# Kernel tuning notes

Hardware: AMD Instinct MI355X
Metric: run time of the kernel (lower is better)

The kernel has to match this reference:

```python
import jax, jax.numpy as jnp
import numpy as np

D_MODEL = 3072
NUM_EXPERTS = 8
TOP_K = 2
BATCH, SEQ = 4, 4096


def setup_inputs() -> dict:
    key = jax.random.key(0)
    kx, kw, kb = jax.random.split(key, 3)
    x = jax.random.normal(kx, (BATCH, SEQ, D_MODEL), dtype=jnp.float32)
    W = jax.random.normal(kw, (NUM_EXPERTS, D_MODEL), dtype=jnp.float32) * (1.0 / np.sqrt(D_MODEL))
    b = jax.random.normal(kb, (NUM_EXPERTS,), dtype=jnp.float32) * 0.02
    return {"x": x, "W": W, "b": b}


def reference(x, W, b):
    # Linear gate: [B, S, D] x [E, D]^T -> [B, S, E]
    logits = jnp.einsum("bsd,ed->bse", x, W) + b
    gate_scores = jax.nn.softmax(logits, axis=-1)
    # top-k over experts
    topk_values, topk_indices = jax.lax.top_k(gate_scores, TOP_K)
    # renormalize the selected scores with a second softmax
    topk_values = jax.nn.softmax(topk_values, axis=-1)
    return (topk_values, topk_indices)
```

## Files before the change

kernel.cpp:

```cpp
#include <hip/hip_runtime.h>
#include <stdint.h>


#define NTOK   16384
#define DMODEL 3072
#define NEXP   8
#define NDB    8
#define DCH    (DMODEL / NDB)
#define DS     32
#define NST    (DCH / DS)
#define TPB    256

__global__ __launch_bounds__(TPB) void gate_logits_kernel(
    const float* __restrict__ x, const float* __restrict__ W,
    float* __restrict__ part) {
  __shared__ float sw[NEXP * DCH];

  const int tid = threadIdx.x;
  const int wv = tid >> 6;
  const int lane = tid & 63;
  const int sl = lane >> 3;
  const int tg = lane & 7;
  const int tokBase = blockIdx.x * TPB;
  const int dBase = blockIdx.y * DCH;

  for (int f = tid; f < NEXP * DCH / 4; f += TPB) {
    const int e = f / (DCH / 4);
    const int j = f - e * (DCH / 4);
    *(float4*)&sw[e * DCH + j * 4] =
        *(const float4*)&W[e * DMODEL + dBase + j * 4];
  }
  __syncthreads();

  const float* p8[8];
#pragma unroll
  for (int p = 0; p < 8; ++p)
    p8[p] = x + (size_t)(tokBase + wv * 64 + p * 8 + tg) * DMODEL + dBase +
            sl * 4;

  float acc[8][NEXP];
#pragma unroll
  for (int p = 0; p < 8; ++p)
#pragma unroll
    for (int e = 0; e < NEXP; ++e) acc[p][e] = 0.f;

  float4 xa[8], xb[8];
#pragma unroll
  for (int p = 0; p < 8; ++p) xa[p] = *(const float4*)(p8[p]);

#pragma unroll 1
  for (int s = 0; s < NST; s += 2) {
#pragma unroll
    for (int p = 0; p < 8; ++p)
      xb[p] = *(const float4*)(p8[p] + (s + 1) * DS);

    float4 w4[NEXP];
#pragma unroll
    for (int e = 0; e < NEXP; ++e)
      w4[e] = *(const float4*)&sw[e * DCH + s * DS + sl * 4];

#pragma unroll
    for (int p = 0; p < 8; ++p) {
      const float4 xv = xa[p];
#pragma unroll
      for (int e = 0; e < NEXP; ++e)
        acc[p][e] = fmaf(xv.x, w4[e].x,
                    fmaf(xv.y, w4[e].y,
                    fmaf(xv.z, w4[e].z,
                    fmaf(xv.w, w4[e].w, acc[p][e]))));
    }

    if (s + 2 < NST) {
#pragma unroll
      for (int p = 0; p < 8; ++p)
        xa[p] = *(const float4*)(p8[p] + (s + 2) * DS);
    }

#pragma unroll
    for (int e = 0; e < NEXP; ++e)
      w4[e] = *(const float4*)&sw[e * DCH + (s + 1) * DS + sl * 4];

#pragma unroll
    for (int p = 0; p < 8; ++p) {
      const float4 xv = xb[p];
#pragma unroll
      for (int e = 0; e < NEXP; ++e)
        acc[p][e] = fmaf(xv.x, w4[e].x,
                    fmaf(xv.y, w4[e].y,
                    fmaf(xv.z, w4[e].z,
                    fmaf(xv.w, w4[e].w, acc[p][e]))));
    }
  }

#pragma unroll
  for (int p = 0; p < 8; ++p)
#pragma unroll
    for (int e = 0; e < NEXP; ++e) {
      float v = acc[p][e];
      v += __shfl_xor(v, 8, 64);
      v += __shfl_xor(v, 16, 64);
      v += __shfl_xor(v, 32, 64);
      acc[p][e] = v;
    }

  float out8[NEXP];
#pragma unroll
  for (int p = 0; p < 8; ++p) {
    if (p == sl) {
#pragma unroll
      for (int e = 0; e < NEXP; ++e) out8[e] = acc[p][e];
    }
  }

  float* op =
      part + ((size_t)blockIdx.y * NTOK + tokBase + wv * 64 + lane) * NEXP;
  *(float4*)op = make_float4(out8[0], out8[1], out8[2], out8[3]);
  *(float4*)(op + 4) = make_float4(out8[4], out8[5], out8[6], out8[7]);
}

__global__ __launch_bounds__(64) void gate_topk_kernel(
    const float* __restrict__ part, const float* __restrict__ bias,
    float* __restrict__ out) {
  const int t = blockIdx.x * 64 + threadIdx.x;
  if (t >= NTOK) return;

  float l[NEXP];
#pragma unroll
  for (int e = 0; e < NEXP; ++e) l[e] = bias[e];
#pragma unroll
  for (int p = 0; p < NDB; ++p) {
    const float* pp = &part[(size_t)p * NTOK * NEXP + (size_t)t * NEXP];
    const float4 a = *(const float4*)pp;
    const float4 b = *(const float4*)(pp + 4);
    l[0] += a.x; l[1] += a.y; l[2] += a.z; l[3] += a.w;
    l[4] += b.x; l[5] += b.y; l[6] += b.z; l[7] += b.w;
  }

  float m = l[0];
#pragma unroll
  for (int e = 1; e < NEXP; ++e) m = fmaxf(m, l[e]);

  float p8[NEXP];
  float ssum = 0.f;
#pragma unroll
  for (int e = 0; e < NEXP; ++e) {
    p8[e] = expf(l[e] - m);
    ssum += p8[e];
  }
  const float inv = 1.f / ssum;
#pragma unroll
  for (int e = 0; e < NEXP; ++e) p8[e] *= inv;

  int i1 = 0;
  float v1 = p8[0];
#pragma unroll
  for (int e = 1; e < NEXP; ++e) {
    if (p8[e] > v1) { v1 = p8[e]; i1 = e; }
  }
  int i2 = -1;
  float v2 = -1.f;
#pragma unroll
  for (int e = 0; e < NEXP; ++e) {
    if (e == i1) continue;
    if (p8[e] > v2) { v2 = p8[e]; i2 = e; }
  }

  const float e2 = expf(v2 - v1);
  const float r = 1.f / (1.f + e2);

  out[(size_t)t * 2 + 0] = r;
  out[(size_t)t * 2 + 1] = e2 * r;
  out[2 * NTOK + (size_t)t * 2 + 0] = (float)i1;
  out[2 * NTOK + (size_t)t * 2 + 1] = (float)i2;
}

extern "C" void kernel_launch(void* const* d_in, const int* in_sizes, int n_in,
                              void* d_out, int out_size, void* d_ws,
                              size_t ws_size, hipStream_t stream) {
  const float* x = (const float*)d_in[0];
  const float* W = (const float*)d_in[1];
  const float* b = (const float*)d_in[2];
  float* out = (float*)d_out;
  float* part = (float*)d_ws;

  dim3 grid1(NTOK / TPB, NDB);
  gate_logits_kernel<<<grid1, TPB, 0, stream>>>(x, W, part);

  gate_topk_kernel<<<NTOK / 64, 64, 0, stream>>>(part, b, out);
}
```

Measured before the change: 286.7 us.

## Fuse gate logits and top-k into one kernel without split-D partials

Replaces the two-kernel split-D scheme (partial logits to workspace, then a reduction plus softmax/top-k kernel) with one fused kernel. Each wavefront now covers 4 tokens across the full model dimension, with 16 lanes per token reduced via shuffles, then does the softmax and top-2 in registers. W is read straight from global memory (cache-resident) instead of staged in LDS. This removes the workspace round trip and the second launch, but drops the per-thread token reuse of W loads, so W load traffic per FMA rises sharply.

```diff
diff --git a/kernel.cpp b/kernel.cpp
--- a/kernel.cpp
+++ b/kernel.cpp
@@ -5,136 +5,96 @@
 #define NTOK   16384
 #define DMODEL 3072
 #define NEXP   8
-#define NDB    8
-#define DCH    (DMODEL / NDB)
-#define DS     32
-#define NST    (DCH / DS)
 #define TPB    256
+#define TOKB   16
+#define NST    48
+#define NSS    12
 
-__global__ __launch_bounds__(TPB) void gate_logits_kernel(
+__global__ __launch_bounds__(TPB) void gate_fused_kernel(
     const float* __restrict__ x, const float* __restrict__ W,
-    float* __restrict__ part) {
-  __shared__ float sw[NEXP * DCH];
-
+    const float* __restrict__ bias, float* __restrict__ out) {
   const int tid = threadIdx.x;
   const int wv = tid >> 6;
   const int lane = tid & 63;
-  const int sl = lane >> 3;
-  const int tg = lane & 7;
-  const int tokBase = blockIdx.x * TPB;
-  const int dBase = blockIdx.y * DCH;
+  const int tg = lane & 3;
+  const int sl = lane >> 2;
+  const int tok = blockIdx.x * TOKB + wv * 4 + tg;
 
-  for (int f = tid; f < NEXP * DCH / 4; f += TPB) {
-    const int e = f / (DCH / 4);
-    const int j = f - e * (DCH / 4);
-    *(float4*)&sw[e * DCH + j * 4] =
-        *(const float4*)&W[e * DMODEL + dBase + j * 4];
-  }
-  __syncthreads();
+  const float* px = x + (size_t)tok * DMODEL + sl * 4;
+  const float* pw[NEXP];
+#pragma unroll
+  for (int e = 0; e < NEXP; ++e) pw[e] = W + (size_t)e * DMODEL + sl * 4;
 
-  const float* p8[8];
+  float acc[NEXP];
 #pragma unroll
-  for (int p = 0; p < 8; ++p)
-    p8[p] = x + (size_t)(tokBase + wv * 64 + p * 8 + tg) * DMODEL + dBase +
-            sl * 4;
+  for (int e = 0; e < NEXP; ++e) acc[e] = 0.f;
 
-  float acc[8][NEXP];
+  float4 xa[4], xb[4];
 #pragma unroll
-  for (int p = 0; p < 8; ++p)
-#pragma unroll
-    for (int e = 0; e < NEXP; ++e) acc[p][e] = 0.f;
-
-  float4 xa[8], xb[8];
-#pragma unroll
-  for (int p = 0; p < 8; ++p) xa[p] = *(const float4*)(p8[p]);
+  for (int k = 0; k < 4; ++k) xa[k] = *(const float4*)(px + k * 64);
 
 #pragma unroll 1
-  for (int s = 0; s < NST; s += 2) {
+  for (int ss = 0; ss < NSS; ss += 2) {
 #pragma unroll
-    for (int p = 0; p < 8; ++p)
-      xb[p] = *(const float4*)(p8[p] + (s + 1) * DS);
-
-    float4 w4[NEXP];
-#pragma unroll
-    for (int e = 0; e < NEXP; ++e)
-      w4[e] = *(const float4*)&sw[e * DCH + s * DS + sl * 4];
+    for (int k = 0; k < 4; ++k)
+      xb[k] = *(const float4*)(px + ((ss + 1) * 4 + k) * 64);
 
 #pragma unroll
-    for (int p = 0; p < 8; ++p) {
-      const float4 xv = xa[p];
+    for (int k = 0; k < 4; ++k) {
+      const int s = ss * 4 + k;
+      float4 w4[NEXP];
 #pragma unroll
       for (int e = 0; e < NEXP; ++e)
-        acc[p][e] = fmaf(xv.x, w4[e].x,
-                    fmaf(xv.y, w4[e].y,
-                    fmaf(xv.z, w4[e].z,
-                    fmaf(xv.w, w4[e].w, acc[p][e]))));
+        w4[e] = *(const float4*)(pw[e] + s * 64);
+      const float4 xv = xa[k];
+#pragma unroll
+      for (int e = 0; e < NEXP; ++e)
+        acc[e] = fmaf(xv.x, w4[e].x,
+                 fmaf(xv.y, w4[e].y,
+                 fmaf(xv.z, w4[e].z,
+                 fmaf(xv.w, w4[e].w, acc[e]))));
     }
 
-    if (s + 2 < NST) {
+    if (ss + 2 < NSS) {
 #pragma unroll
-      for (int p = 0; p < 8; ++p)
-        xa[p] = *(const float4*)(p8[p] + (s + 2) * DS);
+      for (int k = 0; k < 4; ++k)
+        xa[k] = *(const float4*)(px + ((ss + 2) * 4 + k) * 64);
     }
 
 #pragma unroll
-    for (int e = 0; e < NEXP; ++e)
-      w4[e] = *(const float4*)&sw[e * DCH + (s + 1) * DS + sl * 4];
-
-#pragma unroll
-    for (int p = 0; p < 8; ++p) {
-      const float4 xv = xb[p];
+    for (int k = 0; k < 4; ++k) {
+      const int s = (ss + 1) * 4 + k;
+      float4 w4[NEXP];
 #pragma unroll
       for (int e = 0; e < NEXP; ++e)
-        acc[p][e] = fmaf(xv.x, w4[e].x,
-                    fmaf(xv.y, w4[e].y,
-                    fmaf(xv.z, w4[e].z,
-                    fmaf(xv.w, w4[e].w, acc[p][e]))));
+        w4[e] = *(const float4*)(pw[e] + s * 64);
+      const float4 xv = xb[k];
+#pragma unroll
+      for (int e = 0; e < NEXP; ++e)
+        acc[e] = fmaf(xv.x, w4[e].x,
+                 fmaf(xv.y, w4[e].y,
+                 fmaf(xv.z, w4[e].z,
+                 fmaf(xv.w, w4[e].w, acc[e]))));
     }
   }
 
 #pragma unroll
-  for (int p = 0; p < 8; ++p)
-#pragma unroll
-    for (int e = 0; e < NEXP; ++e) {
-      float v = acc[p][e];
-      v += __shfl_xor(v, 8, 64);
-      v += __shfl_xor(v, 16, 64);
-      v += __shfl_xor(v, 32, 64);
-      acc[p][e] = v;
-    }
-
-  float out8[NEXP];
-#pragma unroll
-  for (int p = 0; p < 8; ++p) {
-    if (p == sl) {
-#pragma unroll
-      for (int e = 0; e < NEXP; ++e) out8[e] = acc[p][e];
-    }
+  for (int e = 0; e < NEXP; ++e) {
+    float v = acc[e];
+    v += __shfl_xor(v, 4, 64);
+    v += __shfl_xor(v, 8, 64);
+    v += __shfl_xor(v, 16, 64);
+    v += __shfl_xor(v, 32, 64);
+    acc[e] = v;
   }
 
-  float* op =
-      part + ((size_t)blockIdx.y * NTOK + tokBase + wv * 64 + lane) * NEXP;
-  *(float4*)op = make_float4(out8[0], out8[1], out8[2], out8[3]);
-  *(float4*)(op + 4) = make_float4(out8[4], out8[5], out8[6], out8[7]);
-}
-
-__global__ __launch_bounds__(64) void gate_topk_kernel(
-    const float* __restrict__ part, const float* __restrict__ bias,
-    float* __restrict__ out) {
-  const int t = blockIdx.x * 64 + threadIdx.x;
-  if (t >= NTOK) return;
-
+  const float4 b0 = *(const float4*)bias;
+  const float4 b1 = *(const float4*)(bias + 4);
   float l[NEXP];
-#pragma unroll
-  for (int e = 0; e < NEXP; ++e) l[e] = bias[e];
-#pragma unroll
-  for (int p = 0; p < NDB; ++p) {
-    const float* pp = &part[(size_t)p * NTOK * NEXP + (size_t)t * NEXP];
-    const float4 a = *(const float4*)pp;
-    const float4 b = *(const float4*)(pp + 4);
-    l[0] += a.x; l[1] += a.y; l[2] += a.z; l[3] += a.w;
-    l[4] += b.x; l[5] += b.y; l[6] += b.z; l[7] += b.w;
-  }
+  l[0] = acc[0] + b0.x; l[1] = acc[1] + b0.y;
+  l[2] = acc[2] + b0.z; l[3] = acc[3] + b0.w;
+  l[4] = acc[4] + b1.x; l[5] = acc[5] + b1.y;
+  l[6] = acc[6] + b1.z; l[7] = acc[7] + b1.w;
 
   float m = l[0];
 #pragma unroll
@@ -168,10 +128,11 @@
   const float e2 = expf(v2 - v1);
   const float r = 1.f / (1.f + e2);
 
-  out[(size_t)t * 2 + 0] = r;
-  out[(size_t)t * 2 + 1] = e2 * r;
-  out[2 * NTOK + (size_t)t * 2 + 0] = (float)i1;
-  out[2 * NTOK + (size_t)t * 2 + 1] = (float)i2;
+  if (lane < 4) {
+    *(float2*)(out + (size_t)tok * 2) = make_float2(r, e2 * r);
+    *(float2*)(out + 2 * NTOK + (size_t)tok * 2) =
+        make_float2((float)i1, (float)i2);
+  }
 }
 
 extern "C" void kernel_launch(void* const* d_in, const int* in_sizes, int n_in,
@@ -181,10 +142,7 @@
   const float* W = (const float*)d_in[1];
   const float* b = (const float*)d_in[2];
   float* out = (float*)d_out;
-  float* part = (float*)d_ws;
+  (void)d_ws; (void)ws_size;
 
-  dim3 grid1(NTOK / TPB, NDB);
-  gate_logits_kernel<<<grid1, TPB, 0, stream>>>(x, W, part);
-
-  gate_topk_kernel<<<NTOK / 64, 64, 0, stream>>>(part, b, out);
+  gate_fused_kernel<<<dim3(NTOK / TOKB), TPB, 0, stream>>>(x, W, b, out);
 }
```

New measurement: 307.2 us. 1.07x slower.
